# Kernel optimization log

Hardware: AMD Instinct MI355X
Metric: run time of the kernel (lower is better)

The kernel has to match this reference:

```python
import jax, jax.numpy as jnp
import numpy as np

NUM_IDS = 8
K_HALF = 5            # k = K//2
DIM = 2048
CP_DIM = DIM // 8     # cp_ratio = 8
N = NUM_IDS * 2 * K_HALF
H, W = 24, 8


def _kaiming(key, out_c, in_c):
    # kaiming_normal_(fan_out, relu) for a 1x1 conv: std = sqrt(2/out_c)
    return jax.random.normal(key, (out_c, in_c), dtype=jnp.float32) * np.sqrt(2.0 / out_c)


def setup_inputs() -> dict:
    key = jax.random.key(0)
    ks = jax.random.split(key, 8)
    inputs = jax.random.normal(ks[0], (N, DIM, H, W), dtype=jnp.float32)
    # PK batch: each identity has K_HALF samples with sub==1 and K_HALF with sub==0
    labels = jnp.repeat(jnp.arange(NUM_IDS, dtype=jnp.int64), 2 * K_HALF)
    sub = jnp.tile(jnp.concatenate([jnp.ones(K_HALF, jnp.int64), jnp.zeros(K_HALF, jnp.int64)]), NUM_IDS)
    return {
        "inputs": inputs,
        "labels": labels,
        "sub": sub,
        "W_ri": _kaiming(ks[1], CP_DIM, DIM),
        "W_rv": _kaiming(ks[2], CP_DIM, DIM),
        "W_ci": _kaiming(ks[3], DIM, K_HALF * CP_DIM),
        "W_cv": _kaiming(ks[4], DIM, K_HALF * CP_DIM),
        "W_f": _kaiming(ks[5], DIM, 2 * DIM),
    }


def reference(inputs, labels, sub, W_ri, W_rv, W_ci, W_cv, W_f):
    n, c, h, w = inputs.shape
    cp = W_ri.shape[0]
    k = W_ci.shape[1] // cp
    n_half = n // 2
    x = jax.lax.stop_gradient(inputs)  # .detach() in the original

    def branch(sub_mask_val, Wr, Wc):
        # indices of samples in this sub-group (order-preserving, like boolean mask)
        sidx = jnp.nonzero(sub == sub_mask_val, size=n_half)[0]
        xs = jnp.einsum('nchw,oc->nohw', x[sidx], Wr)       # [n_half, cp, h, w]
        lab = labels[sidx]                                   # [n_half]
        # for each batch sample, the k positions in the sub-group with matching label
        match = labels[:, None] == lab[None, :]              # [n, n_half]
        pos = jnp.where(match, jnp.arange(n_half)[None, :], n_half)
        gidx = jnp.sort(pos, axis=1)[:, :k]                  # [n, k]
        aff = xs[gidx].reshape(n, k * cp, h, w)              # gather + channel-stack
        return jax.nn.relu(jnp.einsum('nchw,oc->nohw', aff, Wc))

    s_i = branch(1, W_ri, W_ci)   # sub == 1
    s_v = branch(0, W_rv, W_cv)   # sub == 0
    x_fuse = jax.nn.sigmoid(
        jnp.einsum('nchw,oc->nohw', jnp.concatenate([s_i, s_v], axis=1), W_f))
    return inputs + inputs * x_fuse
```

## Files before the change

### kernel.cpp

```cpp
#include <hip/hip_runtime.h>

typedef unsigned short u16;
typedef unsigned int u32;
typedef __bf16 bf16_t;
typedef bf16_t bf16x8 __attribute__((ext_vector_type(8)));
typedef float f32x16 __attribute__((ext_vector_type(16)));

#define DIM 2048
#define HW  192
#define CP  256
#define NB  80

__device__ __forceinline__ u16 f2b(float f) {
    u32 u = __float_as_uint(f);
    u32 r = (u + 0x7FFFu + ((u >> 16) & 1u)) >> 16;
    return (u16)r;
}

__device__ __forceinline__ void g2l16(const void* g, void* l) {
    __builtin_amdgcn_global_load_lds(
        (const __attribute__((address_space(1))) u32*)g,
        (__attribute__((address_space(3))) u32*)l, 16, 0, 0);
}

template<int ACT, bool OUTF32, typename F>
__device__ __forceinline__ void gemm_core(F actAddr, int arstride,
    const u16* __restrict__ Wp, int wstride, int K,
    void* __restrict__ outp, int M)
{
    __shared__ u16 act_s[2][96 * 32];
    __shared__ u16 w_s[2][128 * 32];
    const int t    = threadIdx.x;
    const int w    = t >> 6;
    const int lane = t & 63;
    const int ln   = lane & 31;
    const int q2   = lane >> 5;
    const int swz  = (ln >> 1) & 3;

    f32x16 acc[3][2];
    #pragma unroll
    for (int i = 0; i < 3; ++i)
        #pragma unroll
        for (int j = 0; j < 2; ++j)
            #pragma unroll
            for (int r = 0; r < 16; ++r) acc[i][j][r] = 0.f;

    auto stage = [&](int buf, int k0) {
        const u16* ap = actAddr(k0);
        #pragma unroll
        for (int r = 0; r < 4; ++r) {
            int idx = r * 128 + t;
            int row = idx >> 2, pc = idx & 3;
            int lc  = pc ^ ((row >> 1) & 3);
            g2l16(Wp + (size_t)row * wstride + k0 + lc * 8, (void*)(w_s[buf] + idx * 8));
        }
        #pragma unroll
        for (int r = 0; r < 3; ++r) {
            int idx = r * 128 + t;
            int row = idx >> 2, pc = idx & 3;
            int lc  = pc ^ ((row >> 1) & 3);
            g2l16(ap + (size_t)row * arstride + lc * 8, (void*)(act_s[buf] + idx * 8));
        }
    };

    auto compute = [&](int buf) {
        #pragma unroll
        for (int s = 0; s < 2; ++s) {
            bf16x8 af[3], bf[2];
            const int phys = (s * 2 + q2) ^ swz;
            #pragma unroll
            for (int i = 0; i < 3; ++i)
                af[i] = *(const bf16x8*)(act_s[buf] + (i * 32 + ln) * 32 + phys * 8);
            #pragma unroll
            for (int j = 0; j < 2; ++j)
                bf[j] = *(const bf16x8*)(w_s[buf] + (w * 64 + j * 32 + ln) * 32 + phys * 8);
            #pragma unroll
            for (int i = 0; i < 3; ++i)
                #pragma unroll
                for (int j = 0; j < 2; ++j)
                    acc[i][j] = __builtin_amdgcn_mfma_f32_32x32x16_bf16(
                        af[i], bf[j], acc[i][j], 0, 0, 0);
        }
    };

    stage(0, 0);
    const int iters = K / 32;
    for (int it = 0; it < iters; ++it) {
        int b = it & 1;
        __syncthreads();
        if (it + 1 < iters) stage(b ^ 1, (it + 1) * 32);
        compute(b);
    }

    #pragma unroll
    for (int i = 0; i < 3; ++i) {
        #pragma unroll
        for (int j = 0; j < 2; ++j) {
            #pragma unroll
            for (int r = 0; r < 16; ++r) {
                float v = acc[i][j][r];
                if (ACT == 1) v = v > 0.f ? v : 0.f;
                int nl = i * 32 + (r & 3) + 8 * (r >> 2) + 4 * q2;
                int ml = w * 64 + j * 32 + ln;
                if (OUTF32) ((float*)outp)[(size_t)nl * M + ml] = v;
                else        ((u16*)outp)[(size_t)nl * M + ml] = f2b(v);
            }
        }
    }
}

__global__ __launch_bounds__(128) void proj_g(const u16* __restrict__ xt,
    const int* __restrict__ sub, int nbase,
    const u16* __restrict__ Wri, const u16* __restrict__ Wrv,
    float* __restrict__ proj4)
{
    const int zz = blockIdx.z, z = zz >> 2, p = zz & 3;
    const int bn = blockIdx.x, bm = blockIdx.y;
    const int n = nbase + z;
    const u16* act = xt + (size_t)z * (HW * DIM) + (size_t)bn * 96 * DIM + p * 512;
    const u16* Wp  = ((sub[n] != 0) ? Wri : Wrv) + (size_t)bm * 128 * DIM + p * 512;
    float* outp = proj4 + (size_t)p * ((size_t)NB * HW * CP)
                + (size_t)n * (HW * CP) + (size_t)(bn * 96) * CP + bm * 128;
    auto f = [=](int k0) { return act + k0; };
    gemm_core<0, true>(f, DIM, Wp, DIM, 512, outp, CP);
}

__global__ __launch_bounds__(256) void proj_red(const float* __restrict__ proj4,
                                                u16* __restrict__ projt)
{
    const size_t i = ((size_t)blockIdx.x * 256 + threadIdx.x) * 4;
    const size_t S = (size_t)NB * HW * CP;
    float4 a = *(const float4*)(proj4 + i);
    float4 b = *(const float4*)(proj4 + i + S);
    float4 c = *(const float4*)(proj4 + i + 2 * S);
    float4 d = *(const float4*)(proj4 + i + 3 * S);
    ushort4 o;
    o.x = f2b(a.x + b.x + c.x + d.x);
    o.y = f2b(a.y + b.y + c.y + d.y);
    o.z = f2b(a.z + b.z + c.z + d.z);
    o.w = f2b(a.w + b.w + c.w + d.w);
    *(ushort4*)(projt + i) = o;
}

__global__ __launch_bounds__(128) void compose_g(const u16* __restrict__ projt,
    const u16* __restrict__ Wci, const u16* __restrict__ Wcv,
    u16* __restrict__ st)
{
    const int z = blockIdx.z, br = z >> 3, id = z & 7;
    const int bn = blockIdx.x, bm = blockIdx.y;
    const u16* base = projt + (size_t)(id * 10 + br * 5) * (HW * CP) + (size_t)bn * 96 * CP;
    const u16* Wp   = (br ? Wcv : Wci) + (size_t)bm * 128 * 1280;
    u16* outp = st + (size_t)(id * 2 + br) * (HW * DIM) + (size_t)bn * 96 * DIM + bm * 128;
    auto f = [=](int k0) { return base + (size_t)(k0 >> 8) * (HW * CP) + (k0 & 255); };
    gemm_core<1, false>(f, CP, Wp, 1280, 1280, outp, DIM);
}

__global__ __launch_bounds__(128) void fuse_g(const u16* __restrict__ st,
    const u16* __restrict__ Wf, float* __restrict__ fuset4)
{
    const int z = blockIdx.z, h = z >> 3, id = z & 7;
    const int bn = blockIdx.x, bm = blockIdx.y;
    const u16* base = st + (size_t)(id * 2 + (h >> 1)) * (HW * DIM)
                    + (size_t)bn * 96 * DIM + (h & 1) * 1024;
    const u16* Wp   = Wf + (size_t)bm * 128 * (2 * DIM) + (size_t)h * 1024;
    float* outp = fuset4 + (size_t)h * (8 * HW * DIM) + (size_t)id * (HW * DIM)
                + (size_t)bn * 96 * DIM + bm * 128;
    auto f = [=](int k0) { return base + k0; };
    gemm_core<0, true>(f, DIM, Wp, 2 * DIM, 1024, outp, DIM);
}

__global__ __launch_bounds__(256) void xt_k(const float* __restrict__ x,
                                            u16* __restrict__ xt)
{
    __shared__ float ts[64][65];
    const int z = blockIdx.z;
    const int p0 = blockIdx.x * 64, c0 = blockIdx.y * 64;
    const int t = threadIdx.x;
    #pragma unroll
    for (int r = 0; r < 4; ++r) {
        int idx = r * 256 + t;
        int c = idx >> 4, p4 = (idx & 15) * 4;
        float4 v = *(const float4*)(x + ((size_t)z * DIM + c0 + c) * HW + p0 + p4);
        ts[c][p4 + 0] = v.x; ts[c][p4 + 1] = v.y;
        ts[c][p4 + 2] = v.z; ts[c][p4 + 3] = v.w;
    }
    __syncthreads();
    #pragma unroll
    for (int r = 0; r < 4; ++r) {
        int idx = r * 256 + t;
        int p = idx >> 4, c4 = (idx & 15) * 4;
        ushort4 o;
        o.x = f2b(ts[c4 + 0][p]); o.y = f2b(ts[c4 + 1][p]);
        o.z = f2b(ts[c4 + 2][p]); o.w = f2b(ts[c4 + 3][p]);
        *(ushort4*)(xt + ((size_t)z * HW + p0 + p) * DIM + c0 + c4) = o;
    }
}

__global__ __launch_bounds__(256) void fuse_tr(const float* __restrict__ fuset4,
                                               float* __restrict__ fuse)
{
    __shared__ float ts[64][65];
    const int id = blockIdx.z;
    const int c0 = blockIdx.x * 64, p0 = blockIdx.y * 64;
    const int t = threadIdx.x, l = t & 63;
    const size_t hs = (size_t)8 * HW * DIM;
    #pragma unroll
    for (int i = 0; i < 16; ++i) {
        int pl = (t >> 6) * 16 + i;
        size_t a = ((size_t)id * HW + p0 + pl) * DIM + c0 + l;
        float v = fuset4[a] + fuset4[a + hs] + fuset4[a + 2 * hs] + fuset4[a + 3 * hs];
        ts[pl][l] = 1.f / (1.f + __expf(-v));
    }
    __syncthreads();
    #pragma unroll
    for (int i = 0; i < 16; ++i) {
        int cl = (t >> 6) * 16 + i;
        fuse[((size_t)id * DIM + c0 + cl) * HW + p0 + l] = ts[l][cl];
    }
}

__global__ __launch_bounds__(256) void wcvt(
    const float* __restrict__ a0, const float* __restrict__ a1,
    const float* __restrict__ a2, const float* __restrict__ a3,
    const float* __restrict__ a4,
    u16* __restrict__ o0, u16* __restrict__ o1, u16* __restrict__ o2,
    u16* __restrict__ o3, u16* __restrict__ o4)
{
    size_t off = ((size_t)blockIdx.x * 256 + threadIdx.x) * 4;
    const float* s; u16* d;
    if (off < 524288)                    { s = a0; d = o0; }
    else if ((off -= 524288) < 524288)   { s = a1; d = o1; }
    else if ((off -= 524288) < 2621440)  { s = a2; d = o2; }
    else if ((off -= 2621440) < 2621440) { s = a3; d = o3; }
    else                                 { off -= 2621440; s = a4; d = o4; }
    float4 v = *(const float4*)(s + off);
    ushort4 p;
    p.x = f2b(v.x); p.y = f2b(v.y); p.z = f2b(v.z); p.w = f2b(v.w);
    *(ushort4*)(d + off) = p;
}

__global__ __launch_bounds__(256) void final_kernel(const float* __restrict__ x,
    const int* __restrict__ labels, const float* __restrict__ fusebuf,
    float* __restrict__ out)
{
    const u32 e = ((u32)blockIdx.x * 256u + threadIdx.x) * 4u;
    const u32 n   = e / ((u32)DIM * HW);
    const u32 rem = e % ((u32)DIM * HW);
    const int id  = labels[n];
    float4 xv = *reinterpret_cast<const float4*>(x + e);
    float4 fv = *reinterpret_cast<const float4*>(fusebuf + (size_t)id * DIM * HW + rem);
    float4 o;
    o.x = xv.x + xv.x * fv.x;
    o.y = xv.y + xv.y * fv.y;
    o.z = xv.z + xv.z * fv.z;
    o.w = xv.w + xv.w * fv.w;
    *reinterpret_cast<float4*>(out + e) = o;
}

extern "C" void kernel_launch(void* const* d_in, const int* in_sizes, int n_in,
                              void* d_out, int out_size, void* d_ws, size_t ws_size,
                              hipStream_t stream) {
    const float* x      = (const float*)d_in[0];
    const int*   labels = (const int*)d_in[1];
    const int*   sub    = (const int*)d_in[2];
    const float* Wri    = (const float*)d_in[3];
    const float* Wrv    = (const float*)d_in[4];
    const float* Wci    = (const float*)d_in[5];
    const float* Wcv    = (const float*)d_in[6];
    const float* Wf     = (const float*)d_in[7];
    float* out = (float*)d_out;
    char* ws = (char*)d_ws;

    const bool full = ws_size >= (size_t)175636480;
    const size_t xtb = full ? (size_t)62914560 : (size_t)15728640;

    u16* Wri_b = (u16*)(ws);
    u16* Wrv_b = (u16*)(ws + 1048576);
    u16* Wci_b = (u16*)(ws + 2097152);
    u16* Wcv_b = (u16*)(ws + 7340032);
    u16* Wf_b  = (u16*)(ws + 12582912);
    u16* xtbuf = (u16*)(ws + 29360128);
    u16* projt = (u16*)(ws + 29360128 + xtb);
    u16* stb   = (u16*)(ws + 29360128 + xtb + 7864320);
    float* fuset4 = (float*)(ws + 29360128 + xtb + 7864320 + 12582912);
    float* fuse   = (float*)(ws + 29360128 + xtb + 7864320 + 12582912 + 50331648);
    float* proj4 = fuset4;

    wcvt<<<14336, 256, 0, stream>>>(Wri, Wrv, Wci, Wcv, Wf,
                                    Wri_b, Wrv_b, Wci_b, Wcv_b, Wf_b);
    const int nchunk = full ? 1 : 4;
    const int cs = NB / nchunk;
    for (int c = 0; c < nchunk; ++c) {
        xt_k  <<<dim3(3, 32, cs), 256, 0, stream>>>(x + (size_t)c * cs * DIM * HW, xtbuf);
        proj_g<<<dim3(2, 2, cs * 4), 128, 0, stream>>>(xtbuf, sub, c * cs, Wri_b, Wrv_b, proj4);
    }
    proj_red<<<3840, 256, 0, stream>>>(proj4, projt);
    compose_g<<<dim3(2, 16, 16), 128, 0, stream>>>(projt, Wci_b, Wcv_b, stb);
    fuse_g   <<<dim3(2, 16, 32), 128, 0, stream>>>(stb, Wf_b, fuset4);
    fuse_tr  <<<dim3(32, 3, 8), 256, 0, stream>>>(fuset4, fuse);
    final_kernel<<<30720, 256, 0, stream>>>(x, labels, fuse, out);
}
```

Before: 441.5 us.

## Enlarge GEMM block tile to 192x128 with four waves and fuse weight conversion

The shared GEMM core now uses 256-thread blocks arranged as a 2x2 wave grid. Each block covers 192 activation rows (all of HW) by 128 output channels, so the activation tile in LDS is reused across two wave columns. This roughly halves the number of blocks in the proj, compose and fuse GEMMs. The weight fp32-to-bf16 conversion is merged into the transpose kernel (prep_k), which removes one launch and lets the two memory-bound jobs run side by side. In exchange, each GEMM uses more LDS per block and launches fewer blocks, which may lower occupancy and CU fill, for example only 256 blocks in compose.

```diff
diff --git a/kernel.cpp b/kernel.cpp
--- a/kernel.cpp
+++ b/kernel.cpp
@@ -28,10 +28,12 @@
     const u16* __restrict__ Wp, int wstride, int K,
     void* __restrict__ outp, int M)
 {
-    __shared__ u16 act_s[2][96 * 32];
+    __shared__ u16 act_s[2][192 * 32];
     __shared__ u16 w_s[2][128 * 32];
     const int t    = threadIdx.x;
-    const int w    = t >> 6;
+    const int wv   = t >> 6;
+    const int wn   = wv >> 1;
+    const int wm   = wv & 1;
     const int lane = t & 63;
     const int ln   = lane & 31;
     const int q2   = lane >> 5;
@@ -48,15 +50,15 @@
     auto stage = [&](int buf, int k0) {
         const u16* ap = actAddr(k0);
         #pragma unroll
-        for (int r = 0; r < 4; ++r) {
-            int idx = r * 128 + t;
+        for (int r = 0; r < 2; ++r) {
+            int idx = r * 256 + t;
             int row = idx >> 2, pc = idx & 3;
             int lc  = pc ^ ((row >> 1) & 3);
             g2l16(Wp + (size_t)row * wstride + k0 + lc * 8, (void*)(w_s[buf] + idx * 8));
         }
         #pragma unroll
         for (int r = 0; r < 3; ++r) {
-            int idx = r * 128 + t;
+            int idx = r * 256 + t;
             int row = idx >> 2, pc = idx & 3;
             int lc  = pc ^ ((row >> 1) & 3);
             g2l16(ap + (size_t)row * arstride + lc * 8, (void*)(act_s[buf] + idx * 8));
@@ -70,10 +72,10 @@
             const int phys = (s * 2 + q2) ^ swz;
             #pragma unroll
             for (int i = 0; i < 3; ++i)
-                af[i] = *(const bf16x8*)(act_s[buf] + (i * 32 + ln) * 32 + phys * 8);
+                af[i] = *(const bf16x8*)(act_s[buf] + ((wn * 96 + i * 32 + ln) * 32 + phys * 8));
             #pragma unroll
             for (int j = 0; j < 2; ++j)
-                bf[j] = *(const bf16x8*)(w_s[buf] + (w * 64 + j * 32 + ln) * 32 + phys * 8);
+                bf[j] = *(const bf16x8*)(w_s[buf] + ((wm * 64 + j * 32 + ln) * 32 + phys * 8));
             #pragma unroll
             for (int i = 0; i < 3; ++i)
                 #pragma unroll
@@ -100,8 +102,8 @@
             for (int r = 0; r < 16; ++r) {
                 float v = acc[i][j][r];
                 if (ACT == 1) v = v > 0.f ? v : 0.f;
-                int nl = i * 32 + (r & 3) + 8 * (r >> 2) + 4 * q2;
-                int ml = w * 64 + j * 32 + ln;
+                int nl = wn * 96 + i * 32 + (r & 3) + 8 * (r >> 2) + 4 * q2;
+                int ml = wm * 64 + j * 32 + ln;
                 if (OUTF32) ((float*)outp)[(size_t)nl * M + ml] = v;
                 else        ((u16*)outp)[(size_t)nl * M + ml] = f2b(v);
             }
@@ -109,18 +111,18 @@
     }
 }
 
-__global__ __launch_bounds__(128) void proj_g(const u16* __restrict__ xt,
+__global__ __launch_bounds__(256) void proj_g(const u16* __restrict__ xt,
     const int* __restrict__ sub, int nbase,
     const u16* __restrict__ Wri, const u16* __restrict__ Wrv,
     float* __restrict__ proj4)
 {
     const int zz = blockIdx.z, z = zz >> 2, p = zz & 3;
-    const int bn = blockIdx.x, bm = blockIdx.y;
+    const int bm = blockIdx.x;
     const int n = nbase + z;
-    const u16* act = xt + (size_t)z * (HW * DIM) + (size_t)bn * 96 * DIM + p * 512;
+    const u16* act = xt + (size_t)z * (HW * DIM) + p * 512;
     const u16* Wp  = ((sub[n] != 0) ? Wri : Wrv) + (size_t)bm * 128 * DIM + p * 512;
     float* outp = proj4 + (size_t)p * ((size_t)NB * HW * CP)
-                + (size_t)n * (HW * CP) + (size_t)(bn * 96) * CP + bm * 128;
+                + (size_t)n * (HW * CP) + bm * 128;
     auto f = [=](int k0) { return act + k0; };
     gemm_core<0, true>(f, DIM, Wp, DIM, 512, outp, CP);
 }
@@ -142,57 +144,75 @@
     *(ushort4*)(projt + i) = o;
 }
 
-__global__ __launch_bounds__(128) void compose_g(const u16* __restrict__ projt,
+__global__ __launch_bounds__(256) void compose_g(const u16* __restrict__ projt,
     const u16* __restrict__ Wci, const u16* __restrict__ Wcv,
     u16* __restrict__ st)
 {
     const int z = blockIdx.z, br = z >> 3, id = z & 7;
-    const int bn = blockIdx.x, bm = blockIdx.y;
-    const u16* base = projt + (size_t)(id * 10 + br * 5) * (HW * CP) + (size_t)bn * 96 * CP;
+    const int bm = blockIdx.x;
+    const u16* base = projt + (size_t)(id * 10 + br * 5) * (HW * CP);
     const u16* Wp   = (br ? Wcv : Wci) + (size_t)bm * 128 * 1280;
-    u16* outp = st + (size_t)(id * 2 + br) * (HW * DIM) + (size_t)bn * 96 * DIM + bm * 128;
+    u16* outp = st + (size_t)(id * 2 + br) * (HW * DIM) + bm * 128;
     auto f = [=](int k0) { return base + (size_t)(k0 >> 8) * (HW * CP) + (k0 & 255); };
     gemm_core<1, false>(f, CP, Wp, 1280, 1280, outp, DIM);
 }
 
-__global__ __launch_bounds__(128) void fuse_g(const u16* __restrict__ st,
+__global__ __launch_bounds__(256) void fuse_g(const u16* __restrict__ st,
     const u16* __restrict__ Wf, float* __restrict__ fuset4)
 {
     const int z = blockIdx.z, h = z >> 3, id = z & 7;
-    const int bn = blockIdx.x, bm = blockIdx.y;
-    const u16* base = st + (size_t)(id * 2 + (h >> 1)) * (HW * DIM)
-                    + (size_t)bn * 96 * DIM + (h & 1) * 1024;
+    const int bm = blockIdx.x;
+    const u16* base = st + (size_t)(id * 2 + (h >> 1)) * (HW * DIM) + (h & 1) * 1024;
     const u16* Wp   = Wf + (size_t)bm * 128 * (2 * DIM) + (size_t)h * 1024;
-    float* outp = fuset4 + (size_t)h * (8 * HW * DIM) + (size_t)id * (HW * DIM)
-                + (size_t)bn * 96 * DIM + bm * 128;
+    float* outp = fuset4 + (size_t)h * (8 * HW * DIM) + (size_t)id * (HW * DIM) + bm * 128;
     auto f = [=](int k0) { return base + k0; };
     gemm_core<0, true>(f, DIM, Wp, 2 * DIM, 1024, outp, DIM);
 }
 
-__global__ __launch_bounds__(256) void xt_k(const float* __restrict__ x,
-                                            u16* __restrict__ xt)
+__global__ __launch_bounds__(256) void prep_k(const float* __restrict__ x,
+    u16* __restrict__ xt, int nxt, int wc,
+    const float* __restrict__ a0, const float* __restrict__ a1,
+    const float* __restrict__ a2, const float* __restrict__ a3,
+    const float* __restrict__ a4,
+    u16* __restrict__ o0, u16* __restrict__ o1, u16* __restrict__ o2,
+    u16* __restrict__ o3, u16* __restrict__ o4)
 {
     __shared__ float ts[64][65];
-    const int z = blockIdx.z;
-    const int p0 = blockIdx.x * 64, c0 = blockIdx.y * 64;
+    const int b = blockIdx.x;
     const int t = threadIdx.x;
-    #pragma unroll
-    for (int r = 0; r < 4; ++r) {
-        int idx = r * 256 + t;
-        int c = idx >> 4, p4 = (idx & 15) * 4;
-        float4 v = *(const float4*)(x + ((size_t)z * DIM + c0 + c) * HW + p0 + p4);
-        ts[c][p4 + 0] = v.x; ts[c][p4 + 1] = v.y;
-        ts[c][p4 + 2] = v.z; ts[c][p4 + 3] = v.w;
-    }
-    __syncthreads();
-    #pragma unroll
-    for (int r = 0; r < 4; ++r) {
-        int idx = r * 256 + t;
-        int p = idx >> 4, c4 = (idx & 15) * 4;
-        ushort4 o;
-        o.x = f2b(ts[c4 + 0][p]); o.y = f2b(ts[c4 + 1][p]);
-        o.z = f2b(ts[c4 + 2][p]); o.w = f2b(ts[c4 + 3][p]);
-        *(ushort4*)(xt + ((size_t)z * HW + p0 + p) * DIM + c0 + c4) = o;
+    if (b < nxt) {
+        const int z = b / 96, r6 = b % 96;
+        const int p0 = (r6 % 3) * 64, c0 = (r6 / 3) * 64;
+        #pragma unroll
+        for (int r = 0; r < 4; ++r) {
+            int idx = r * 256 + t;
+            int c = idx >> 4, p4 = (idx & 15) * 4;
+            float4 v = *(const float4*)(x + ((size_t)z * DIM + c0 + c) * HW + p0 + p4);
+            ts[c][p4 + 0] = v.x; ts[c][p4 + 1] = v.y;
+            ts[c][p4 + 2] = v.z; ts[c][p4 + 3] = v.w;
+        }
+        __syncthreads();
+        #pragma unroll
+        for (int r = 0; r < 4; ++r) {
+            int idx = r * 256 + t;
+            int p = idx >> 4, c4 = (idx & 15) * 4;
+            ushort4 o;
+            o.x = f2b(ts[c4 + 0][p]); o.y = f2b(ts[c4 + 1][p]);
+            o.z = f2b(ts[c4 + 2][p]); o.w = f2b(ts[c4 + 3][p]);
+            *(ushort4*)(xt + ((size_t)z * HW + p0 + p) * DIM + c0 + c4) = o;
+        }
+    } else if (wc) {
+        size_t off = ((size_t)(b - nxt) * 256 + t) * 4;
+        const float* s; u16* d;
+        if (off < 524288)                    { s = a0; d = o0; }
+        else if ((off -= 524288) < 524288)   { s = a1; d = o1; }
+        else if ((off -= 524288) < 2621440)  { s = a2; d = o2; }
+        else if ((off -= 2621440) < 2621440) { s = a3; d = o3; }
+        else                                 { off -= 2621440; s = a4; d = o4; }
+        float4 v = *(const float4*)(s + off);
+        ushort4 p;
+        p.x = f2b(v.x); p.y = f2b(v.y); p.z = f2b(v.z); p.w = f2b(v.w);
+        *(ushort4*)(d + off) = p;
     }
 }
 
@@ -217,26 +237,6 @@
         int cl = (t >> 6) * 16 + i;
         fuse[((size_t)id * DIM + c0 + cl) * HW + p0 + l] = ts[l][cl];
     }
-}
-
-__global__ __launch_bounds__(256) void wcvt(
-    const float* __restrict__ a0, const float* __restrict__ a1,
-    const float* __restrict__ a2, const float* __restrict__ a3,
-    const float* __restrict__ a4,
-    u16* __restrict__ o0, u16* __restrict__ o1, u16* __restrict__ o2,
-    u16* __restrict__ o3, u16* __restrict__ o4)
-{
-    size_t off = ((size_t)blockIdx.x * 256 + threadIdx.x) * 4;
-    const float* s; u16* d;
-    if (off < 524288)                    { s = a0; d = o0; }
-    else if ((off -= 524288) < 524288)   { s = a1; d = o1; }
-    else if ((off -= 524288) < 2621440)  { s = a2; d = o2; }
-    else if ((off -= 2621440) < 2621440) { s = a3; d = o3; }
-    else                                 { off -= 2621440; s = a4; d = o4; }
-    float4 v = *(const float4*)(s + off);
-    ushort4 p;
-    p.x = f2b(v.x); p.y = f2b(v.y); p.z = f2b(v.z); p.w = f2b(v.w);
-    *(ushort4*)(d + off) = p;
 }
 
 __global__ __launch_bounds__(256) void final_kernel(const float* __restrict__ x,
@@ -286,17 +286,19 @@
     float* fuse   = (float*)(ws + 29360128 + xtb + 7864320 + 12582912 + 50331648);
     float* proj4 = fuset4;
 
-    wcvt<<<14336, 256, 0, stream>>>(Wri, Wrv, Wci, Wcv, Wf,
-                                    Wri_b, Wrv_b, Wci_b, Wcv_b, Wf_b);
     const int nchunk = full ? 1 : 4;
     const int cs = NB / nchunk;
     for (int c = 0; c < nchunk; ++c) {
-        xt_k  <<<dim3(3, 32, cs), 256, 0, stream>>>(x + (size_t)c * cs * DIM * HW, xtbuf);
-        proj_g<<<dim3(2, 2, cs * 4), 128, 0, stream>>>(xtbuf, sub, c * cs, Wri_b, Wrv_b, proj4);
+        const int nxt = 96 * cs;
+        const int wc = (c == 0) ? 1 : 0;
+        prep_k<<<nxt + (wc ? 14336 : 0), 256, 0, stream>>>(
+            x + (size_t)c * cs * DIM * HW, xtbuf, nxt, wc,
+            Wri, Wrv, Wci, Wcv, Wf, Wri_b, Wrv_b, Wci_b, Wcv_b, Wf_b);
+        proj_g<<<dim3(2, 1, cs * 4), 256, 0, stream>>>(xtbuf, sub, c * cs, Wri_b, Wrv_b, proj4);
     }
     proj_red<<<3840, 256, 0, stream>>>(proj4, projt);
-    compose_g<<<dim3(2, 16, 16), 128, 0, stream>>>(projt, Wci_b, Wcv_b, stb);
-    fuse_g   <<<dim3(2, 16, 32), 128, 0, stream>>>(stb, Wf_b, fuset4);
+    compose_g<<<dim3(16, 1, 16), 256, 0, stream>>>(projt, Wci_b, Wcv_b, stb);
+    fuse_g   <<<dim3(16, 1, 32), 256, 0, stream>>>(stb, Wf_b, fuset4);
     fuse_tr  <<<dim3(32, 3, 8), 256, 0, stream>>>(fuset4, fuse);
     final_kernel<<<30720, 256, 0, stream>>>(x, labels, fuse, out);
 }
```

New measurement: 426.0 us. 3.5% less time.
